# Optimization experiments

Measured on AMD Instinct MI355X. Metric: run time of the kernel, lower is better.

The kernel has to match this reference:

```python
import jax, jax.numpy as jnp
import numpy as np

B, L, N, DOUT = 8, 8192, 256, 256  # batch, seq_len, state_dim, output_dim


def setup_inputs() -> dict:
    key = jax.random.key(0)
    k_u, k_h, k_w = jax.random.split(key, 3)
    u = jax.random.normal(k_u, (B, L, 1), dtype=jnp.float32)
    # impulse response buffer (stands in for A_bar^i @ B_bar rows); decay-scaled for realism
    h = jax.random.normal(k_h, (L, N), dtype=jnp.float32) * 0.02
    W = jax.random.normal(k_w, (DOUT, N), dtype=jnp.float32) * (1.0 / np.sqrt(N))
    return {"u": u, "h": h, "W": W}


def reference(u, h, W):
    L_ = h.shape[0]
    n_fft = 2 * L_
    # FFT-based long convolution: U:[B, n_fft//2+1, 1], H:[n_fft//2+1, N]
    U = jnp.fft.rfft(u, n=n_fft, axis=1)
    H = jnp.fft.rfft(h, n=n_fft, axis=0)
    M = U * H[None, :, :]                      # broadcast channel 1 -> N
    m = jnp.fft.irfft(M, n=n_fft, axis=1)[:, :L_, :]  # [B, L, N]
    return jnp.einsum('bln,on->blo', m, W)     # Linear(state_dim -> output_dim), no bias
```

## Files before the change

kernel.cpp:

```cpp
#include <hip/hip_runtime.h>
#include <hip/hip_bf16.h>
#include <stdint.h>
#include <stddef.h>

typedef __attribute__((ext_vector_type(4))) float f32x4;
typedef __attribute__((ext_vector_type(8))) short s16x8;

#define B_    8
#define L_    8192
#define N_    256
#define DOUT_ 256

__device__ __forceinline__ unsigned short f2bf(float f) {
  unsigned int x = __float_as_uint(f);
  x += 0x7fff + ((x >> 16) & 1);
  return (unsigned short)(x >> 16);
}

__global__ void k_convert(const float* __restrict__ h, const float* __restrict__ W,
                          unsigned short* __restrict__ hb, unsigned short* __restrict__ Wb) {
  int t = blockIdx.x * 256 + threadIdx.x;
  int base = t * 4;
  const int TH = L_ * N_;
  const int TW = DOUT_ * N_;
  if (base < TH) {
    float4 v = *(const float4*)(h + base);
    hb[base + 0] = f2bf(v.x); hb[base + 1] = f2bf(v.y);
    hb[base + 2] = f2bf(v.z); hb[base + 3] = f2bf(v.w);
  } else if (base < TH + TW) {
    int wb = base - TH;
    float4 v = *(const float4*)(W + wb);
    Wb[wb + 0] = f2bf(v.x); Wb[wb + 1] = f2bf(v.y);
    Wb[wb + 2] = f2bf(v.z); Wb[wb + 3] = f2bf(v.w);
  }
}

__global__ void k_amat(const float* __restrict__ u, unsigned short* __restrict__ Am) {
  int t = blockIdx.x * 256 + threadIdx.x;
  int i0 = (t & 15) * 8;
  int lp = (t >> 4) & 127;
  int r2 = t >> 11;
  int d  = r2 % 65;
  int b  = r2 / 65;
  s16x8 v;
#pragma unroll
  for (int j = 0; j < 8; ++j) v[j] = 0;
  if (d < 64) {
    const float* ub = u + b * L_;
    int base = 128 * d + lp - i0;
#pragma unroll
    for (int j = 0; j < 8; ++j) {
      int idx = base - j;
      float f = (idx >= 0) ? ub[idx] : 0.0f;
      v[j] = (short)f2bf(f);
    }
  }
  *(s16x8*)(Am + (size_t)t * 8) = v;
}

__global__ void k_gt(const unsigned short* __restrict__ Wb, const unsigned short* __restrict__ hb,
                     unsigned short* __restrict__ gT) {
  int gid  = blockIdx.x * 256 + threadIdx.x;
  int lane = gid & 63;
  int wid  = gid >> 6;
  int o_t  = wid >> 7;
  int i_t  = wid & 127;
  int o0 = o_t * 16, i0 = i_t * 64;
  int ln = lane & 15, hi = lane >> 4;
  f32x4 acc[4] = {};
#pragma unroll
  for (int k0 = 0; k0 < N_; k0 += 32) {
    s16x8 a = *(const s16x8*)(Wb + (o0 + ln) * N_ + k0 + 8 * hi);
#pragma unroll
    for (int ns = 0; ns < 4; ++ns) {
      s16x8 bfr = *(const s16x8*)(hb + (i0 + 16 * ns + ln) * N_ + k0 + 8 * hi);
      acc[ns] = __builtin_amdgcn_mfma_f32_16x16x32_bf16(a, bfr, acc[ns], 0, 0, 0);
    }
  }
#pragma unroll
  for (int ns = 0; ns < 4; ++ns)
#pragma unroll
    for (int q = 0; q < 4; ++q)
      gT[(size_t)(o0 + 4 * hi + q) * L_ + i0 + 16 * ns + ln] = f2bf(acc[ns][q]);
}

__global__ __launch_bounds__(512, 2) void k_main(const unsigned short* __restrict__ Am,
                                                 const unsigned short* __restrict__ gT,
                                                 float* __restrict__ out) {
  __shared__ short As[2][16384];
  __shared__ short Bs[2][8192];
  const int c = blockIdx.x;
  const int b = blockIdx.y;
  const int R = 31 - blockIdx.z;
  const int tid = threadIdx.x;
  const int lane = tid & 63;
  const int w = tid >> 6;
  const int wr = w >> 1, wc = w & 1;
  const int ln = lane & 15, hi = lane >> 4;
  const int ob = c * 128;

  const int t3 = tid >> 3;
  const int sA = ((tid & 7) ^ (t3 & 7)) << 3;
  const unsigned short* AmB = Am + (size_t)(b * 65) * 16384;
  const unsigned short* Bb0 = gT + (size_t)(ob + t3) * L_ + sA;
  const unsigned short* Bb1 = gT + (size_t)(ob + t3 + 64) * L_ + sA;
  const int rl0 = t3;
  const int rl1 = 64 + t3;

  const int offA = (wr * 64 + ln) * 64;
  const int offB = (wc * 64 + ln) * 64;
  const int sw = ln & 7;
  const int off_k0 = (hi ^ sw) * 8;
  const int off_k1 = ((hi + 4) ^ sw) * 8;

  f32x4 acc[4][4] = {};
  const int nkt = 4 * (R + 1);

#define ISSUE_A(ktv, buf) do { \
    const int kthalf_ = (ktv) >> 1; const int kodd_ = ((ktv) & 1) << 6; \
    _Pragma("unroll") \
    for (int q = 0; q < 4; ++q) { \
      int dd = 2 * R + (q >> 1) - kthalf_; \
      int sd = dd < 0 ? 64 : dd; \
      const unsigned short* src = AmB + ((size_t)sd << 14) + ((q & 1 ? rl1 : rl0) << 7) + kodd_ + sA; \
      __builtin_amdgcn_global_load_lds((const __attribute__((address_space(1))) void*)src, \
          (__attribute__((address_space(3))) void*)(&As[buf][(tid + 512 * q) * 8]), 16, 0, 0); \
    } \
  } while (0)

#define ISSUE_B(ktv, buf) do { \
    const int kb_ = (ktv) * 64; \
    __builtin_amdgcn_global_load_lds((const __attribute__((address_space(1))) void*)(Bb0 + kb_), \
        (__attribute__((address_space(3))) void*)(&Bs[buf][tid * 8]), 16, 0, 0); \
    __builtin_amdgcn_global_load_lds((const __attribute__((address_space(1))) void*)(Bb1 + kb_), \
        (__attribute__((address_space(3))) void*)(&Bs[buf][(tid + 512) * 8]), 16, 0, 0); \
  } while (0)

  ISSUE_A(0, 0);
  ISSUE_B(0, 0);

  for (int kt = 0; kt < nkt; ++kt) {
    const int cur = kt & 1;
    const int nxt = cur ^ 1;
    const int kt1 = (kt + 1 < nkt) ? kt + 1 : kt;

    ISSUE_A(kt1, nxt);
    asm volatile("s_waitcnt vmcnt(4)" ::: "memory");
    __builtin_amdgcn_sched_barrier(0);
    __builtin_amdgcn_s_barrier();
    __builtin_amdgcn_sched_barrier(0);
    const short* Ac = &As[cur][0];
    const short* Bc = &Bs[cur][0];
    s16x8 af[4][2], bf[2][2];
#pragma unroll
    for (int m = 0; m < 4; ++m) {
      af[m][0] = *(const s16x8*)(Ac + offA + m * 1024 + off_k0);
      af[m][1] = *(const s16x8*)(Ac + offA + m * 1024 + off_k1);
    }
#pragma unroll
    for (int n = 0; n < 2; ++n) {
      bf[n][0] = *(const s16x8*)(Bc + offB + n * 1024 + off_k0);
      bf[n][1] = *(const s16x8*)(Bc + offB + n * 1024 + off_k1);
    }
    __builtin_amdgcn_s_setprio(1);
#pragma unroll
    for (int kk = 0; kk < 2; ++kk)
#pragma unroll
      for (int m = 0; m < 4; ++m)
#pragma unroll
        for (int n = 0; n < 2; ++n)
          acc[m][n] = __builtin_amdgcn_mfma_f32_16x16x32_bf16(af[m][kk], bf[n][kk], acc[m][n], 0, 0, 0);
    __builtin_amdgcn_s_setprio(0);

    ISSUE_B(kt1, nxt);
    s16x8 bg[2][2];
#pragma unroll
    for (int n = 0; n < 2; ++n) {
      bg[n][0] = *(const s16x8*)(Bc + offB + (n + 2) * 1024 + off_k0);
      bg[n][1] = *(const s16x8*)(Bc + offB + (n + 2) * 1024 + off_k1);
    }
    __builtin_amdgcn_s_setprio(1);
#pragma unroll
    for (int kk = 0; kk < 2; ++kk)
#pragma unroll
      for (int m = 0; m < 4; ++m)
#pragma unroll
        for (int n = 0; n < 2; ++n)
          acc[m][n + 2] = __builtin_amdgcn_mfma_f32_16x16x32_bf16(af[m][kk], bg[n][kk], acc[m][n + 2], 0, 0, 0);
    __builtin_amdgcn_s_setprio(0);
    __builtin_amdgcn_sched_barrier(0);
    __builtin_amdgcn_s_barrier();
    __builtin_amdgcn_sched_barrier(0);
  }

  asm volatile("s_waitcnt vmcnt(0)" ::: "memory");

  const int l0 = R * 256 + wr * 64 + 4 * hi;
  const int o0 = ob + wc * 64 + ln;
  float* outb = out + (size_t)b * L_ * DOUT_;
#pragma unroll
  for (int m = 0; m < 4; ++m)
#pragma unroll
    for (int q = 0; q < 4; ++q) {
      float* rowp = outb + (size_t)(l0 + m * 16 + q) * DOUT_ + o0;
#pragma unroll
      for (int n = 0; n < 4; ++n)
        rowp[n * 16] = acc[m][n][q];
    }
#undef ISSUE_A
#undef ISSUE_B
}

extern "C" void kernel_launch(void* const* d_in, const int* in_sizes, int n_in,
                              void* d_out, int out_size, void* d_ws, size_t ws_size,
                              hipStream_t stream) {
  const float* u = (const float*)d_in[0];
  const float* h = (const float*)d_in[1];
  const float* W = (const float*)d_in[2];
  float* out = (float*)d_out;

  char* ws = (char*)d_ws;
  const size_t AM_BYTES = (size_t)8 * 65 * 16384 * 2;
  unsigned short* Am = (unsigned short*)ws;
  unsigned short* gT = (unsigned short*)(ws + AM_BYTES);
  unsigned short* Wb = (unsigned short*)(ws + AM_BYTES + (size_t)4 * 1024 * 1024);
  unsigned short* hb = (unsigned short*)ws;

  k_convert<<<2112, 256, 0, stream>>>(h, W, hb, Wb);
  k_gt<<<512, 256, 0, stream>>>(Wb, hb, gT);
  k_amat<<<4160, 256, 0, stream>>>(u, Am);
  k_main<<<dim3(2, 8, 32), 512, 0, stream>>>(Am, gT, out);
}
```

Measured before the change: 201.0 us.

## Fuse bf16 conversion into gT GEMM, triple-buffer main loop, pair causal tiles per block

Drops the separate conversion kernel: k_gt now reads fp32 W and h directly and converts to bf16 in registers, removing one launch and a pass over h. The main kernel moves from double to triple buffering in LDS with a prefetch distance of two and one barrier per k-step instead of two. Each block now processes two row tiles (R=31-z and R=z), so every block does the same amount of triangular work and the grid halves. Triple buffering raises LDS use to about 144KB per block, which likely cuts occupancy below the two blocks per CU requested by launch bounds.

```diff
diff --git a/kernel.cpp b/kernel.cpp
--- a/kernel.cpp
+++ b/kernel.cpp
@@ -15,24 +15,6 @@
   unsigned int x = __float_as_uint(f);
   x += 0x7fff + ((x >> 16) & 1);
   return (unsigned short)(x >> 16);
-}
-
-__global__ void k_convert(const float* __restrict__ h, const float* __restrict__ W,
-                          unsigned short* __restrict__ hb, unsigned short* __restrict__ Wb) {
-  int t = blockIdx.x * 256 + threadIdx.x;
-  int base = t * 4;
-  const int TH = L_ * N_;
-  const int TW = DOUT_ * N_;
-  if (base < TH) {
-    float4 v = *(const float4*)(h + base);
-    hb[base + 0] = f2bf(v.x); hb[base + 1] = f2bf(v.y);
-    hb[base + 2] = f2bf(v.z); hb[base + 3] = f2bf(v.w);
-  } else if (base < TH + TW) {
-    int wb = base - TH;
-    float4 v = *(const float4*)(W + wb);
-    Wb[wb + 0] = f2bf(v.x); Wb[wb + 1] = f2bf(v.y);
-    Wb[wb + 2] = f2bf(v.z); Wb[wb + 3] = f2bf(v.w);
-  }
 }
 
 __global__ void k_amat(const float* __restrict__ u, unsigned short* __restrict__ Am) {
@@ -58,7 +40,7 @@
   *(s16x8*)(Am + (size_t)t * 8) = v;
 }
 
-__global__ void k_gt(const unsigned short* __restrict__ Wb, const unsigned short* __restrict__ hb,
+__global__ void k_gt(const float* __restrict__ W, const float* __restrict__ h,
                      unsigned short* __restrict__ gT) {
   int gid  = blockIdx.x * 256 + threadIdx.x;
   int lane = gid & 63;
@@ -70,11 +52,25 @@
   f32x4 acc[4] = {};
 #pragma unroll
   for (int k0 = 0; k0 < N_; k0 += 32) {
-    s16x8 a = *(const s16x8*)(Wb + (o0 + ln) * N_ + k0 + 8 * hi);
+    const float* wp = W + (o0 + ln) * N_ + k0 + 8 * hi;
+    float4 w0 = *(const float4*)wp;
+    float4 w1 = *(const float4*)(wp + 4);
+    s16x8 a;
+    a[0] = (short)f2bf(w0.x); a[1] = (short)f2bf(w0.y);
+    a[2] = (short)f2bf(w0.z); a[3] = (short)f2bf(w0.w);
+    a[4] = (short)f2bf(w1.x); a[5] = (short)f2bf(w1.y);
+    a[6] = (short)f2bf(w1.z); a[7] = (short)f2bf(w1.w);
 #pragma unroll
     for (int ns = 0; ns < 4; ++ns) {
-      s16x8 bfr = *(const s16x8*)(hb + (i0 + 16 * ns + ln) * N_ + k0 + 8 * hi);
-      acc[ns] = __builtin_amdgcn_mfma_f32_16x16x32_bf16(a, bfr, acc[ns], 0, 0, 0);
+      const float* hp = h + (size_t)(i0 + 16 * ns + ln) * N_ + k0 + 8 * hi;
+      float4 h0 = *(const float4*)hp;
+      float4 h1 = *(const float4*)(hp + 4);
+      s16x8 bb;
+      bb[0] = (short)f2bf(h0.x); bb[1] = (short)f2bf(h0.y);
+      bb[2] = (short)f2bf(h0.z); bb[3] = (short)f2bf(h0.w);
+      bb[4] = (short)f2bf(h1.x); bb[5] = (short)f2bf(h1.y);
+      bb[6] = (short)f2bf(h1.z); bb[7] = (short)f2bf(h1.w);
+      acc[ns] = __builtin_amdgcn_mfma_f32_16x16x32_bf16(a, bb, acc[ns], 0, 0, 0);
     }
   }
 #pragma unroll
@@ -87,11 +83,11 @@
 __global__ __launch_bounds__(512, 2) void k_main(const unsigned short* __restrict__ Am,
                                                  const unsigned short* __restrict__ gT,
                                                  float* __restrict__ out) {
-  __shared__ short As[2][16384];
-  __shared__ short Bs[2][8192];
+  __shared__ short As[3][16384];
+  __shared__ short Bs[3][8192];
   const int c = blockIdx.x;
   const int b = blockIdx.y;
-  const int R = 31 - blockIdx.z;
+  const int z = blockIdx.z;
   const int tid = threadIdx.x;
   const int lane = tid & 63;
   const int w = tid >> 6;
@@ -113,100 +109,108 @@
   const int off_k0 = (hi ^ sw) * 8;
   const int off_k1 = ((hi + 4) ^ sw) * 8;
 
-  f32x4 acc[4][4] = {};
-  const int nkt = 4 * (R + 1);
-
-#define ISSUE_A(ktv, buf) do { \
+  float* outb = out + (size_t)b * L_ * DOUT_;
+
+#define ISSUE_A(Rv, ktv, dst) do { \
     const int kthalf_ = (ktv) >> 1; const int kodd_ = ((ktv) & 1) << 6; \
     _Pragma("unroll") \
     for (int q = 0; q < 4; ++q) { \
-      int dd = 2 * R + (q >> 1) - kthalf_; \
+      int dd = 2 * (Rv) + (q >> 1) - kthalf_; \
       int sd = dd < 0 ? 64 : dd; \
       const unsigned short* src = AmB + ((size_t)sd << 14) + ((q & 1 ? rl1 : rl0) << 7) + kodd_ + sA; \
       __builtin_amdgcn_global_load_lds((const __attribute__((address_space(1))) void*)src, \
-          (__attribute__((address_space(3))) void*)(&As[buf][(tid + 512 * q) * 8]), 16, 0, 0); \
+          (__attribute__((address_space(3))) void*)((dst) + (tid + 512 * q) * 8), 16, 0, 0); \
     } \
   } while (0)
 
-#define ISSUE_B(ktv, buf) do { \
+#define ISSUE_B(ktv, dst) do { \
     const int kb_ = (ktv) * 64; \
     __builtin_amdgcn_global_load_lds((const __attribute__((address_space(1))) void*)(Bb0 + kb_), \
-        (__attribute__((address_space(3))) void*)(&Bs[buf][tid * 8]), 16, 0, 0); \
+        (__attribute__((address_space(3))) void*)((dst) + tid * 8), 16, 0, 0); \
     __builtin_amdgcn_global_load_lds((const __attribute__((address_space(1))) void*)(Bb1 + kb_), \
-        (__attribute__((address_space(3))) void*)(&Bs[buf][(tid + 512) * 8]), 16, 0, 0); \
+        (__attribute__((address_space(3))) void*)((dst) + (tid + 512) * 8), 16, 0, 0); \
   } while (0)
 
-  ISSUE_A(0, 0);
-  ISSUE_B(0, 0);
-
-  for (int kt = 0; kt < nkt; ++kt) {
-    const int cur = kt & 1;
-    const int nxt = cur ^ 1;
-    const int kt1 = (kt + 1 < nkt) ? kt + 1 : kt;
-
-    ISSUE_A(kt1, nxt);
-    asm volatile("s_waitcnt vmcnt(4)" ::: "memory");
-    __builtin_amdgcn_sched_barrier(0);
+  auto run_section = [&](const int R) {
+    short *ar = &As[0][0], *an = &As[1][0], *aw = &As[2][0];
+    short *br = &Bs[0][0], *bn = &Bs[1][0], *bw = &Bs[2][0];
+    f32x4 acc[4][4] = {};
+    const int nkt = 4 * (R + 1);
+
+    ISSUE_A(R, 0, ar); ISSUE_B(0, br);
+    ISSUE_A(R, 1, an); ISSUE_B(1, bn);
+
+    for (int kt = 0; kt < nkt; ++kt) {
+      asm volatile("s_waitcnt vmcnt(6)" ::: "memory");
+      __builtin_amdgcn_sched_barrier(0);
+      __builtin_amdgcn_s_barrier();
+      __builtin_amdgcn_sched_barrier(0);
+
+      const int kt2 = (kt + 2 < nkt) ? kt + 2 : nkt - 1;
+
+      s16x8 af[4][2], bf[2][2];
+#pragma unroll
+      for (int m = 0; m < 4; ++m) {
+        af[m][0] = *(const s16x8*)(ar + offA + m * 1024 + off_k0);
+        af[m][1] = *(const s16x8*)(ar + offA + m * 1024 + off_k1);
+      }
+#pragma unroll
+      for (int n = 0; n < 2; ++n) {
+        bf[n][0] = *(const s16x8*)(br + offB + n * 1024 + off_k0);
+        bf[n][1] = *(const s16x8*)(br + offB + n * 1024 + off_k1);
+      }
+      ISSUE_A(R, kt2, aw);
+      __builtin_amdgcn_s_setprio(1);
+#pragma unroll
+      for (int kk = 0; kk < 2; ++kk)
+#pragma unroll
+        for (int m = 0; m < 4; ++m)
+#pragma unroll
+          for (int n = 0; n < 2; ++n)
+            acc[m][n] = __builtin_amdgcn_mfma_f32_16x16x32_bf16(af[m][kk], bf[n][kk], acc[m][n], 0, 0, 0);
+      __builtin_amdgcn_s_setprio(0);
+
+      s16x8 bg[2][2];
+#pragma unroll
+      for (int n = 0; n < 2; ++n) {
+        bg[n][0] = *(const s16x8*)(br + offB + (n + 2) * 1024 + off_k0);
+        bg[n][1] = *(const s16x8*)(br + offB + (n + 2) * 1024 + off_k1);
+      }
+      ISSUE_B(kt2, bw);
+      __builtin_amdgcn_s_setprio(1);
+#pragma unroll
+      for (int kk = 0; kk < 2; ++kk)
+#pragma unroll
+        for (int m = 0; m < 4; ++m)
+#pragma unroll
+          for (int n = 0; n < 2; ++n)
+            acc[m][n + 2] = __builtin_amdgcn_mfma_f32_16x16x32_bf16(af[m][kk], bg[n][kk], acc[m][n + 2], 0, 0, 0);
+      __builtin_amdgcn_s_setprio(0);
+
+      short* t;
+      t = ar; ar = an; an = aw; aw = t;
+      t = br; br = bn; bn = bw; bw = t;
+    }
+
     __builtin_amdgcn_s_barrier();
-    __builtin_amdgcn_sched_barrier(0);
-    const short* Ac = &As[cur][0];
-    const short* Bc = &Bs[cur][0];
-    s16x8 af[4][2], bf[2][2];
-#pragma unroll
-    for (int m = 0; m < 4; ++m) {
-      af[m][0] = *(const s16x8*)(Ac + offA + m * 1024 + off_k0);
-      af[m][1] = *(const s16x8*)(Ac + offA + m * 1024 + off_k1);
-    }
-#pragma unroll
-    for (int n = 0; n < 2; ++n) {
-      bf[n][0] = *(const s16x8*)(Bc + offB + n * 1024 + off_k0);
-      bf[n][1] = *(const s16x8*)(Bc + offB + n * 1024 + off_k1);
-    }
-    __builtin_amdgcn_s_setprio(1);
-#pragma unroll
-    for (int kk = 0; kk < 2; ++kk)
-#pragma unroll
-      for (int m = 0; m < 4; ++m)
-#pragma unroll
-        for (int n = 0; n < 2; ++n)
-          acc[m][n] = __builtin_amdgcn_mfma_f32_16x16x32_bf16(af[m][kk], bf[n][kk], acc[m][n], 0, 0, 0);
-    __builtin_amdgcn_s_setprio(0);
-
-    ISSUE_B(kt1, nxt);
-    s16x8 bg[2][2];
-#pragma unroll
-    for (int n = 0; n < 2; ++n) {
-      bg[n][0] = *(const s16x8*)(Bc + offB + (n + 2) * 1024 + off_k0);
-      bg[n][1] = *(const s16x8*)(Bc + offB + (n + 2) * 1024 + off_k1);
-    }
-    __builtin_amdgcn_s_setprio(1);
-#pragma unroll
-    for (int kk = 0; kk < 2; ++kk)
-#pragma unroll
-      for (int m = 0; m < 4; ++m)
-#pragma unroll
-        for (int n = 0; n < 2; ++n)
-          acc[m][n + 2] = __builtin_amdgcn_mfma_f32_16x16x32_bf16(af[m][kk], bg[n][kk], acc[m][n + 2], 0, 0, 0);
-    __builtin_amdgcn_s_setprio(0);
-    __builtin_amdgcn_sched_barrier(0);
-    __builtin_amdgcn_s_barrier();
-    __builtin_amdgcn_sched_barrier(0);
-  }
-
-  asm volatile("s_waitcnt vmcnt(0)" ::: "memory");
-
-  const int l0 = R * 256 + wr * 64 + 4 * hi;
-  const int o0 = ob + wc * 64 + ln;
-  float* outb = out + (size_t)b * L_ * DOUT_;
-#pragma unroll
-  for (int m = 0; m < 4; ++m)
-#pragma unroll
-    for (int q = 0; q < 4; ++q) {
-      float* rowp = outb + (size_t)(l0 + m * 16 + q) * DOUT_ + o0;
-#pragma unroll
-      for (int n = 0; n < 4; ++n)
-        rowp[n * 16] = acc[m][n][q];
-    }
+    asm volatile("s_waitcnt vmcnt(0)" ::: "memory");
+
+    const int l0 = R * 256 + wr * 64 + 4 * hi;
+    const int o0 = ob + wc * 64 + ln;
+#pragma unroll
+    for (int m = 0; m < 4; ++m)
+#pragma unroll
+      for (int q = 0; q < 4; ++q) {
+        float* rowp = outb + (size_t)(l0 + m * 16 + q) * DOUT_ + o0;
+#pragma unroll
+        for (int n = 0; n < 4; ++n)
+          rowp[n * 16] = acc[m][n][q];
+      }
+  };
+
+  run_section(31 - z);
+  run_section(z);
+
 #undef ISSUE_A
 #undef ISSUE_B
 }
@@ -223,11 +227,8 @@
   const size_t AM_BYTES = (size_t)8 * 65 * 16384 * 2;
   unsigned short* Am = (unsigned short*)ws;
   unsigned short* gT = (unsigned short*)(ws + AM_BYTES);
-  unsigned short* Wb = (unsigned short*)(ws + AM_BYTES + (size_t)4 * 1024 * 1024);
-  unsigned short* hb = (unsigned short*)ws;
-
-  k_convert<<<2112, 256, 0, stream>>>(h, W, hb, Wb);
-  k_gt<<<512, 256, 0, stream>>>(Wb, hb, gT);
+
   k_amat<<<4160, 256, 0, stream>>>(u, Am);
-  k_main<<<dim3(2, 8, 32), 512, 0, stream>>>(Am, gT, out);
-}
+  k_gt<<<512, 256, 0, stream>>>(W, h, gT);
+  k_main<<<dim3(2, 8, 16), 512, 0, stream>>>(Am, gT, out);
+}
```

Result: faster. 176.7 us (-12.1%).
